# Kernel tuning notes

Measured on AMD Instinct MI355X. Metric: run time of the kernel, lower is better.

Reference implementation:

```python
import jax, jax.numpy as jnp
import numpy as np
from jax import lax

R = 2            # search_range
S = 2 * R + 1    # window extent per axis
NCH = S ** 3     # output channels (125)


def _offset_table():
    # Loop order matches the original triple loop (i over H, j over W, h over D).
    # Channel index (S*i + S*j + h) may be negative -> Python negative indexing,
    starts, chans = [], []
    for i in range(-R, R + 1):          # H shift
        for j in range(-R, R + 1):      # W shift
            for h in range(-R, R + 1):  # D shift
                # out[a] = sum_c x1[a] * x2[a - shift]; padded start = R - shift
                starts.append((R - h, R - i, R - j))
                chans.append((S * i + S * j + h) % NCH)
    src = np.full(NCH, -1, dtype=np.int64)
    for t, c in enumerate(chans):
        src[c] = t
    return np.asarray(starts, np.int32), src


def setup_inputs() -> dict:
    key = jax.random.key(0)
    k1, k2 = jax.random.split(key)
    B, C, D, H, W = 2, 64, 32, 64, 64
    x1 = jax.random.normal(k1, (B, C, D, H, W), dtype=jnp.float32)
    x2 = jax.random.normal(k2, (B, C, D, H, W), dtype=jnp.float32)
    return {"x1": x1, "x2": x2}


def reference(x1, x2):
    B, C, D, H, W = x1.shape
    starts_np, src_np = _offset_table()
    starts = jnp.asarray(starts_np)                          # [NCH, 3]
    # zero-pad x2 so every shifted window is a static-size slice
    x2p = jnp.pad(x2, ((0, 0), (0, 0), (R, R), (R, R), (R, R)))

    def corr(off):
        x2s = lax.dynamic_slice(x2p, (0, 0, off[0], off[1], off[2]),
                                (B, C, D, H, W))
        return jnp.einsum('bcdhw,bcdhw->bdhw', x1, x2s)

    corrs = lax.map(corr, starts)                            # [NCH, B, D, H, W]
    src = jnp.asarray(src_np)
    written = (src >= 0)[:, None, None, None, None]
    cv = jnp.where(written, corrs[jnp.clip(src, 0)], jnp.float32(0.0))
    return jnp.transpose(cv, (1, 0, 2, 3, 4)) / NCH          # [B, NCH, D, H, W]
```

## Files before the change

### kernel.cpp

```cpp
#include <hip/hip_runtime.h>

#define B_ 2
#define C_ 64
#define D_ 32
#define H_ 64
#define W_ 64
#define NCH 125
#define HW_ 4096
#define DHW_ 131072
#define CDHW_ 8388608

#define TROWS 8
#define TBUF (TROWS * W_)
#define WREG (3 * TBUF)

typedef float f32x4 __attribute__((ext_vector_type(4)));

__device__ __attribute__((aligned(16))) const float g_zero[4] = {0.f, 0.f, 0.f, 0.f};

__device__ __forceinline__ void glds16(const float* g, float* l) {
    __builtin_amdgcn_global_load_lds(
        (const __attribute__((address_space(1))) void*)g,
        (__attribute__((address_space(3))) void*)l, 16, 0, 0);
}

__device__ __forceinline__ void nt_store4(float* p, float a, float b,
                                          float c, float d) {
    f32x4 v = {a, b, c, d};
    __builtin_nontemporal_store(v, (f32x4*)p);
}

__global__ __launch_bounds__(128, 5) void cv_all(const float* __restrict__ x1,
                                                 const float* __restrict__ x2,
                                                 float* __restrict__ out)
{
    __shared__ __align__(16) float lds[4 + 2 * WREG + 4];

    const int tid  = threadIdx.y * 16 + threadIdx.x;
    const int lane = tid & 63;
    const int w    = tid >> 6;
    const int tx   = lane & 15;
    const int lr0  = lane >> 4;

    const int lin     = blockIdx.x;
    const int logical = (lin & 7) * 320 + (lin >> 3);
    const int bz   = logical % 10;
    const int rest = logical / 10;
    const int y0   = (rest & 7) * 8;
    const int d    = rest >> 3;
    const int b    = bz / 5;
    const int hi   = bz - b * 5;
    const int hh   = hi - 2;
    const int y0w  = y0 + 4 * w;
    const int y    = y0w + lr0;
    const int x    = tx * 4;
    const int zd   = d - hh;
    const bool zok = (zd >= 0) && (zd < D_);

    const float* x2b = x2 + (size_t)b * CDHW_ + (size_t)(zok ? zd : 0) * HW_;
    const int q   = lane & 15;
    const int grA = y0w - 2 + (lane >> 4);
    const int grB = y0w + 2 + (lane >> 4);
    const bool vA = zok && (grA >= 0);
    const bool vB = zok && (grB < H_);
    const float* pA = vA ? (x2b + grA * W_ + 4 * q) : g_zero;
    const float* pB = vB ? (x2b + grB * W_ + 4 * q) : g_zero;
    const int sA = vA ? DHW_ : 0;
    const int sB = vB ? DHW_ : 0;

    const int wbase = 4 + w * WREG;
    const float* p1 = x1 + (size_t)b * CDHW_ + (size_t)d * HW_ + (y * W_ + x);

    float* obz = out + (size_t)b * NCH * DHW_ + (size_t)(23 + hi * 16) * DHW_
                     + (size_t)d * HW_ + (y * W_ + x);

    glds16(pA, lds + wbase);
    glds16(pB, lds + wbase + TBUF / 2);
    float4 a0 = *(const float4*)p1;
    pA += sA; pB += sB;

    float acc[9][4];
#pragma unroll
    for (int k = 0; k < 9; ++k)
#pragma unroll
        for (int j = 0; j < 4; ++j) acc[k][j] = 0.f;

    const bool lo_edge = (tx == 0);
    const bool hi_edge = (tx == 15);

#pragma unroll 2
    for (int c = 0; c < C_; ++c) {
        float* dst = lds + wbase + ((c + 1) % 3) * TBUF;
        glds16(pA, dst);
        glds16(pB, dst + TBUF / 2);
        float4 a1 = *(const float4*)(p1 + (size_t)((c + 1) & 63) * DHW_);
        if (c < 62) { pA += sA; pB += sB; }

        asm volatile("s_waitcnt vmcnt(3)" ::: "memory");

        const float* Bb = lds + wbase + (c % 3) * TBUF;
        const float4 a = a0;
        float2 k0A, k0B;
#pragma unroll
        for (int k = 0; k < 5; ++k) {
            const float* pr = Bb + (lr0 + k) * W_ + x;
            const float2 cA = *(const float2*)(pr + 2);
            float2 cB = *(const float2*)(pr + 4);
            cB.x = hi_edge ? 0.f : cB.x;
            cB.y = hi_edge ? 0.f : cB.y;
            if (k == 0) { k0A = cA; k0B = cB; }
            const int ai = 4 - k;
            acc[ai][0] += a.x * cA.x;
            acc[ai][1] += a.y * cA.y;
            acc[ai][2] += a.z * cB.x;
            acc[ai][3] += a.w * cB.y;
        }
        {
            const float* pr = Bb + lr0 * W_ + x;
            float2 rlA = *(const float2*)(pr - 2);
            const float2 rlB = *(const float2*)(pr);
            rlA.x = lo_edge ? 0.f : rlA.x;
            rlA.y = lo_edge ? 0.f : rlA.y;
            const float r8[8] = {rlA.x, rlA.y, rlB.x, rlB.y,
                                 k0A.x, k0A.y, k0B.x, k0B.y};
#pragma unroll
            for (int s = 1; s <= 4; ++s) {
                const int ai = s + 4;
                acc[ai][0] += a.x * r8[4 - s];
                acc[ai][1] += a.y * r8[5 - s];
                acc[ai][2] += a.z * r8[6 - s];
                acc[ai][3] += a.w * r8[7 - s];
            }
        }
        a0 = a1;

        if ((c & 3) == 0)
            nt_store4(obz + (size_t)(c >> 2) * DHW_, 0.f, 0.f, 0.f, 0.f);
    }

    float* ob = out + (size_t)b * NCH * DHW_ + (size_t)d * HW_ + (y * W_ + x);
    const float inv = 1.0f / 125.0f;
#pragma unroll
    for (int k = 0; k < 9; ++k) {
        const int s = k - 4;
        int ch = 5 * s + hh;
        ch = (ch % NCH + NCH) % NCH;
        nt_store4(ob + (size_t)ch * DHW_,
                  acc[k][0] * inv, acc[k][1] * inv,
                  acc[k][2] * inv, acc[k][3] * inv);
    }
}

extern "C" void kernel_launch(void* const* d_in, const int* in_sizes, int n_in,
                              void* d_out, int out_size, void* d_ws, size_t ws_size,
                              hipStream_t stream) {
    const float* x1 = (const float*)d_in[0];
    const float* x2 = (const float*)d_in[1];
    float* out = (float*)d_out;
    cv_all<<<dim3(2560, 1, 1), dim3(16, 8, 1), 0, stream>>>(x1, x2, out);
}
```

Measured before the change: 267.2 us.

## Replace LDS-staged x2 tiles with direct per-thread global loads and register prefetch

```diff
diff --git a/kernel.cpp b/kernel.cpp
--- a/kernel.cpp
+++ b/kernel.cpp
@@ -10,19 +10,8 @@
 #define DHW_ 131072
 #define CDHW_ 8388608
 
-#define TROWS 8
-#define TBUF (TROWS * W_)
-#define WREG (3 * TBUF)
 
 typedef float f32x4 __attribute__((ext_vector_type(4)));
-
-__device__ __attribute__((aligned(16))) const float g_zero[4] = {0.f, 0.f, 0.f, 0.f};
-
-__device__ __forceinline__ void glds16(const float* g, float* l) {
-    __builtin_amdgcn_global_load_lds(
-        (const __attribute__((address_space(1))) void*)g,
-        (__attribute__((address_space(3))) void*)l, 16, 0, 0);
-}
 
 __device__ __forceinline__ void nt_store4(float* p, float a, float b,
                                           float c, float d) {
@@ -30,12 +19,10 @@
     __builtin_nontemporal_store(v, (f32x4*)p);
 }
 
-__global__ __launch_bounds__(128, 5) void cv_all(const float* __restrict__ x1,
+__global__ __launch_bounds__(128, 4) void cv_all(const float* __restrict__ x1,
                                                  const float* __restrict__ x2,
                                                  float* __restrict__ out)
 {
-    __shared__ __align__(16) float lds[4 + 2 * WREG + 4];
-
     const int tid  = threadIdx.y * 16 + threadIdx.x;
     const int lane = tid & 63;
     const int w    = tid >> 6;
@@ -51,33 +38,51 @@
     const int b    = bz / 5;
     const int hi   = bz - b * 5;
     const int hh   = hi - 2;
-    const int y0w  = y0 + 4 * w;
-    const int y    = y0w + lr0;
+    const int y    = y0 + 4 * w + lr0;
     const int x    = tx * 4;
     const int zd   = d - hh;
     const bool zok = (zd >= 0) && (zd < D_);
+    const bool lo_edge = (tx == 0);
+    const bool hi_edge = (tx == 15);
 
-    const float* x2b = x2 + (size_t)b * CDHW_ + (size_t)(zok ? zd : 0) * HW_;
-    const int q   = lane & 15;
-    const int grA = y0w - 2 + (lane >> 4);
-    const int grB = y0w + 2 + (lane >> 4);
-    const bool vA = zok && (grA >= 0);
-    const bool vB = zok && (grB < H_);
-    const float* pA = vA ? (x2b + grA * W_ + 4 * q) : g_zero;
-    const float* pB = vB ? (x2b + grB * W_ + 4 * q) : g_zero;
-    const int sA = vA ? DHW_ : 0;
-    const int sB = vB ? DHW_ : 0;
+    const int zdc = zok ? zd : 0;
+    const float* xb2 = x2 + (size_t)b * CDHW_;
+    const float* xb1 = x1 + (size_t)b * CDHW_;
 
-    const int wbase = 4 + w * WREG;
-    const float* p1 = x1 + (size_t)b * CDHW_ + (size_t)d * HW_ + (y * W_ + x);
+    bool mRow[5], mB[5];
+    int  offA[5], offB[5];
+    const int colB = hi_edge ? 60 : (x + 4);
+#pragma unroll
+    for (int k = 0; k < 5; ++k) {
+        const int yy  = y - 2 + k;
+        mRow[k] = zok && (yy >= 0) && (yy < H_);
+        mB[k]   = mRow[k] && !hi_edge;
+        const int yyc = yy < 0 ? 0 : (yy > 63 ? 63 : yy);
+        offA[k] = zdc * HW_ + yyc * W_ + (x + 2);
+        offB[k] = zdc * HW_ + yyc * W_ + colB;
+    }
+    const bool mLB = mRow[0];
+    const bool mLA = mRow[0] && !lo_edge;
+    const int yyc0 = (y - 2) < 0 ? 0 : (y - 2);
+    int offLA = zdc * HW_ + yyc0 * W_ + (lo_edge ? 0 : (x - 2));
+
+    int off1 = d * HW_ + y * W_ + x;
 
     float* obz = out + (size_t)b * NCH * DHW_ + (size_t)(23 + hi * 16) * DHW_
                      + (size_t)d * HW_ + (y * W_ + x);
 
-    glds16(pA, lds + wbase);
-    glds16(pB, lds + wbase + TBUF / 2);
-    float4 a0 = *(const float4*)p1;
-    pA += sA; pB += sB;
+    float2 cA[5], cB[5];
+#pragma unroll
+    for (int k = 0; k < 5; ++k) {
+        cA[k] = *(const float2*)(xb2 + offA[k]);
+        cB[k] = *(const float2*)(xb2 + offB[k]);
+    }
+    float2 cLA = *(const float2*)(xb2 + offLA);
+    float2 cLB = *(const float2*)(xb2 + offA[0] - 2);
+    float4 a0  = *(const float4*)(xb1 + off1);
+#pragma unroll
+    for (int k = 0; k < 5; ++k) { offA[k] += DHW_; offB[k] += DHW_; }
+    offLA += DHW_; off1 += DHW_;
 
     float acc[9][4];
 #pragma unroll
@@ -85,44 +90,44 @@
 #pragma unroll
         for (int j = 0; j < 4; ++j) acc[k][j] = 0.f;
 
-    const bool lo_edge = (tx == 0);
-    const bool hi_edge = (tx == 15);
-
 #pragma unroll 2
     for (int c = 0; c < C_; ++c) {
-        float* dst = lds + wbase + ((c + 1) % 3) * TBUF;
-        glds16(pA, dst);
-        glds16(pB, dst + TBUF / 2);
-        float4 a1 = *(const float4*)(p1 + (size_t)((c + 1) & 63) * DHW_);
-        if (c < 62) { pA += sA; pB += sB; }
-
-        asm volatile("s_waitcnt vmcnt(3)" ::: "memory");
-
-        const float* Bb = lds + wbase + (c % 3) * TBUF;
-        const float4 a = a0;
-        float2 k0A, k0B;
+        float2 nA[5], nB[5];
 #pragma unroll
         for (int k = 0; k < 5; ++k) {
-            const float* pr = Bb + (lr0 + k) * W_ + x;
-            const float2 cA = *(const float2*)(pr + 2);
-            float2 cB = *(const float2*)(pr + 4);
-            cB.x = hi_edge ? 0.f : cB.x;
-            cB.y = hi_edge ? 0.f : cB.y;
-            if (k == 0) { k0A = cA; k0B = cB; }
+            nA[k] = *(const float2*)(xb2 + offA[k]);
+            nB[k] = *(const float2*)(xb2 + offB[k]);
+        }
+        float2 nLA = *(const float2*)(xb2 + offLA);
+        float2 nLB = *(const float2*)(xb2 + offA[0] - 2);
+        float4 na  = *(const float4*)(xb1 + off1);
+        if (c < 62) {
+#pragma unroll
+            for (int k = 0; k < 5; ++k) { offA[k] += DHW_; offB[k] += DHW_; }
+            offLA += DHW_; off1 += DHW_;
+        }
+
+        const float4 a = a0;
+        float k0A0, k0A1, k0B0, k0B1;
+#pragma unroll
+        for (int k = 0; k < 5; ++k) {
+            const float vA0 = mRow[k] ? cA[k].x : 0.f;
+            const float vA1 = mRow[k] ? cA[k].y : 0.f;
+            const float vB0 = mB[k]   ? cB[k].x : 0.f;
+            const float vB1 = mB[k]   ? cB[k].y : 0.f;
+            if (k == 0) { k0A0 = vA0; k0A1 = vA1; k0B0 = vB0; k0B1 = vB1; }
             const int ai = 4 - k;
-            acc[ai][0] += a.x * cA.x;
-            acc[ai][1] += a.y * cA.y;
-            acc[ai][2] += a.z * cB.x;
-            acc[ai][3] += a.w * cB.y;
+            acc[ai][0] += a.x * vA0;
+            acc[ai][1] += a.y * vA1;
+            acc[ai][2] += a.z * vB0;
+            acc[ai][3] += a.w * vB1;
         }
         {
-            const float* pr = Bb + lr0 * W_ + x;
-            float2 rlA = *(const float2*)(pr - 2);
-            const float2 rlB = *(const float2*)(pr);
-            rlA.x = lo_edge ? 0.f : rlA.x;
-            rlA.y = lo_edge ? 0.f : rlA.y;
-            const float r8[8] = {rlA.x, rlA.y, rlB.x, rlB.y,
-                                 k0A.x, k0A.y, k0B.x, k0B.y};
+            const float rl0 = mLA ? cLA.x : 0.f;
+            const float rl1 = mLA ? cLA.y : 0.f;
+            const float rl2 = mLB ? cLB.x : 0.f;
+            const float rl3 = mLB ? cLB.y : 0.f;
+            const float r8[8] = {rl0, rl1, rl2, rl3, k0A0, k0A1, k0B0, k0B1};
 #pragma unroll
             for (int s = 1; s <= 4; ++s) {
                 const int ai = s + 4;
@@ -132,7 +137,10 @@
                 acc[ai][3] += a.w * r8[7 - s];
             }
         }
-        a0 = a1;
+
+#pragma unroll
+        for (int k = 0; k < 5; ++k) { cA[k] = nA[k]; cB[k] = nB[k]; }
+        cLA = nLA; cLB = nLB; a0 = na;
 
         if ((c & 3) == 0)
             nt_store4(obz + (size_t)(c >> 2) * DHW_, 0.f, 0.f, 0.f, 0.f);
```

Result: slower. 368.1 us (+37.8%).

## Split channel reduction across two waves and reduce partial sums through LDS

Applied to the files above, without the earlier changes.

```diff
diff --git a/kernel.cpp b/kernel.cpp
--- a/kernel.cpp
+++ b/kernel.cpp
@@ -12,7 +12,7 @@
 
 #define TROWS 8
 #define TBUF (TROWS * W_)
-#define WREG (3 * TBUF)
+#define WREG (2 * TBUF + 4)
 
 typedef float f32x4 __attribute__((ext_vector_type(4)));
 
@@ -30,11 +30,11 @@
     __builtin_nontemporal_store(v, (f32x4*)p);
 }
 
-__global__ __launch_bounds__(128, 5) void cv_all(const float* __restrict__ x1,
+__global__ __launch_bounds__(128, 8) void cv_all(const float* __restrict__ x1,
                                                  const float* __restrict__ x2,
                                                  float* __restrict__ out)
 {
-    __shared__ __align__(16) float lds[4 + 2 * WREG + 4];
+    __shared__ __align__(16) float lds[2304];
 
     const int tid  = threadIdx.y * 16 + threadIdx.x;
     const int lane = tid & 63;
@@ -43,24 +43,25 @@
     const int lr0  = lane >> 4;
 
     const int lin     = blockIdx.x;
-    const int logical = (lin & 7) * 320 + (lin >> 3);
+    const int logical = (lin & 7) * 640 + (lin >> 3);
     const int bz   = logical % 10;
     const int rest = logical / 10;
-    const int y0   = (rest & 7) * 8;
-    const int d    = rest >> 3;
+    const int y0   = (rest & 15) * 4;
+    const int d    = rest >> 4;
     const int b    = bz / 5;
     const int hi   = bz - b * 5;
     const int hh   = hi - 2;
-    const int y0w  = y0 + 4 * w;
-    const int y    = y0w + lr0;
+    const int y    = y0 + lr0;
     const int x    = tx * 4;
     const int zd   = d - hh;
     const bool zok = (zd >= 0) && (zd < D_);
+    const int c0   = w << 5;
 
-    const float* x2b = x2 + (size_t)b * CDHW_ + (size_t)(zok ? zd : 0) * HW_;
-    const int q   = lane & 15;
-    const int grA = y0w - 2 + (lane >> 4);
-    const int grB = y0w + 2 + (lane >> 4);
+    const float* x2b = x2 + (size_t)b * CDHW_ + (size_t)c0 * DHW_
+                          + (size_t)(zok ? zd : 0) * HW_;
+    const int q   = tx;
+    const int grA = y0 - 2 + lr0;
+    const int grB = y0 + 2 + lr0;
     const bool vA = zok && (grA >= 0);
     const bool vB = zok && (grB < H_);
     const float* pA = vA ? (x2b + grA * W_ + 4 * q) : g_zero;
@@ -69,7 +70,8 @@
     const int sB = vB ? DHW_ : 0;
 
     const int wbase = 4 + w * WREG;
-    const float* p1 = x1 + (size_t)b * CDHW_ + (size_t)d * HW_ + (y * W_ + x);
+    const float* p1 = x1 + (size_t)b * CDHW_ + (size_t)c0 * DHW_
+                         + (size_t)d * HW_ + (y * W_ + x);
 
     float* obz = out + (size_t)b * NCH * DHW_ + (size_t)(23 + hi * 16) * DHW_
                      + (size_t)d * HW_ + (y * W_ + x);
@@ -89,16 +91,16 @@
     const bool hi_edge = (tx == 15);
 
 #pragma unroll 2
-    for (int c = 0; c < C_; ++c) {
-        float* dst = lds + wbase + ((c + 1) % 3) * TBUF;
+    for (int c = 0; c < 32; ++c) {
+        float* dst = lds + wbase + ((c + 1) & 1) * TBUF;
         glds16(pA, dst);
         glds16(pB, dst + TBUF / 2);
-        float4 a1 = *(const float4*)(p1 + (size_t)((c + 1) & 63) * DHW_);
-        if (c < 62) { pA += sA; pB += sB; }
+        float4 a1 = *(const float4*)(p1 + (size_t)((c + 1) & 31) * DHW_);
+        if (c < 30) { pA += sA; pB += sB; }
 
         asm volatile("s_waitcnt vmcnt(3)" ::: "memory");
 
-        const float* Bb = lds + wbase + (c % 3) * TBUF;
+        const float* Bb = lds + wbase + (c & 1) * TBUF;
         const float4 a = a0;
         float2 k0A, k0B;
 #pragma unroll
@@ -135,13 +137,45 @@
         a0 = a1;
 
         if ((c & 3) == 0)
-            nt_store4(obz + (size_t)(c >> 2) * DHW_, 0.f, 0.f, 0.f, 0.f);
+            nt_store4(obz + (size_t)(w * 8 + (c >> 2)) * DHW_,
+                      0.f, 0.f, 0.f, 0.f);
+    }
+
+    __syncthreads();
+    if (w == 1) {
+#pragma unroll
+        for (int k = 0; k < 5; ++k)
+#pragma unroll
+            for (int j = 0; j < 4; ++j)
+                lds[lane * 20 + k * 4 + j] = acc[k][j];
+    }
+    __syncthreads();
+    if (w == 0) {
+#pragma unroll
+        for (int k = 0; k < 5; ++k)
+#pragma unroll
+            for (int j = 0; j < 4; ++j)
+                acc[k][j] += lds[lane * 20 + k * 4 + j];
+#pragma unroll
+        for (int k = 5; k < 9; ++k)
+#pragma unroll
+            for (int j = 0; j < 4; ++j)
+                lds[1280 + lane * 16 + (k - 5) * 4 + j] = acc[k][j];
+    }
+    __syncthreads();
+    if (w == 1) {
+#pragma unroll
+        for (int k = 5; k < 9; ++k)
+#pragma unroll
+            for (int j = 0; j < 4; ++j)
+                acc[k][j] += lds[1280 + lane * 16 + (k - 5) * 4 + j];
     }
 
     float* ob = out + (size_t)b * NCH * DHW_ + (size_t)d * HW_ + (y * W_ + x);
     const float inv = 1.0f / 125.0f;
-#pragma unroll
-    for (int k = 0; k < 9; ++k) {
+    const int kBeg = (w == 0) ? 0 : 5;
+    const int kEnd = (w == 0) ? 5 : 9;
+    for (int k = kBeg; k < kEnd; ++k) {
         const int s = k - 4;
         int ch = 5 * s + hh;
         ch = (ch % NCH + NCH) % NCH;
@@ -157,5 +191,5 @@
     const float* x1 = (const float*)d_in[0];
     const float* x2 = (const float*)d_in[1];
     float* out = (float*)d_out;
-    cv_all<<<dim3(2560, 1, 1), dim3(16, 8, 1), 0, stream>>>(x1, x2, out);
+    cv_all<<<dim3(5120, 1, 1), dim3(16, 8, 1), 0, stream>>>(x1, x2, out);
 }
```

New measurement: 738.8 us. +176.5%, slower.
